# Kernel optimization log

Measured on AMD Instinct MI355X. Metric: run time of the kernel, lower is better.

Reference implementation:

```python
import jax, jax.numpy as jnp
import numpy as np

N_DRUG, N_CELL, N_EDGES = 10000, 20000, 1280000
D_DRUG, D_CELL, BATCH = 384, 3504, 4096


def setup_inputs() -> dict:
    key = jax.random.key(0)
    ks = jax.random.split(key, 24)
    f32 = jnp.float32

    def lin(kw, kb, fan_in, fan_out, bias=True):
        s = 1.0 / np.sqrt(fan_in)
        W = jax.random.uniform(kw, (fan_in, fan_out), f32, -s, s)
        b = jax.random.uniform(kb, (fan_out,), f32, -s, s) if bias else None
        return W, b

    inp = {}
    inp['drug'] = jax.random.randint(ks[0], (BATCH,), 0, N_DRUG)
    inp['cell'] = jax.random.randint(ks[1], (BATCH,), 0, N_CELL)
    # stored node features / edges (constants in the torch module)
    inp['drug_x'] = jax.random.normal(ks[2], (N_DRUG, D_DRUG), f32)
    inp['cell_x'] = jax.random.normal(ks[3], (N_CELL, D_CELL), f32)
    inp['cell_edges'] = jax.random.randint(ks[4], (2, N_EDGES), 0, N_CELL)
    # drug_emb: Linear(384,128)
    inp['demb_W'], inp['demb_b'] = lin(ks[5], ks[6], D_DRUG, 128)
    # SAGEConv(3504,1024): lin_l (with bias) on aggregated, lin_r (no bias) on root
    inp['c1_lW'], inp['c1_lb'] = lin(ks[7], ks[8], D_CELL, 1024)
    inp['c1_rW'], _ = lin(ks[9], ks[9], D_CELL, 1024, bias=False)
    # SAGEConv(1024,256)
    inp['c2_lW'], inp['c2_lb'] = lin(ks[10], ks[11], 1024, 256)
    inp['c2_rW'], _ = lin(ks[12], ks[12], 1024, 256, bias=False)
    inp['reg_W1'], inp['reg_b1'] = lin(ks[13], ks[14], 384, 384)
    inp['reg_W2'], inp['reg_b2'] = lin(ks[15], ks[16], 384, 384)
    inp['reg_W3'], inp['reg_b3'] = lin(ks[17], ks[18], 384, 1)
    return inp


def _sage(x, src, dst, n, lW, lb, rW):
    # PyG SAGEConv, mean aggregation: lin_l(mean_{j in N(i)} x_j) + lin_r(x_i)
    deg = jax.ops.segment_sum(jnp.ones(src.shape[0], x.dtype), dst, num_segments=n)
    agg = jax.ops.segment_sum(x[src], dst, num_segments=n)  # [n, d_in]
    agg = agg / jnp.maximum(deg, 1.0)[:, None]
    return agg @ lW + lb + x @ rW


def reference(drug, cell, drug_x, cell_x, cell_edges,
              demb_W, demb_b, c1_lW, c1_lb, c1_rW, c2_lW, c2_lb, c2_rW,
              reg_W1, reg_b1, reg_W2, reg_b2, reg_W3, reg_b3):
    src, dst = cell_edges[0], cell_edges[1]
    n = cell_x.shape[0]
    # drug branch: Linear + ReLU (dropout = identity at inference)
    d = jax.nn.relu(drug_x @ demb_W + demb_b)                  # [N_drug, 128]
    # cell branch: two SAGEConv + ReLU
    c = jax.nn.relu(_sage(cell_x, src, dst, n, c1_lW, c1_lb, c1_rW))  # [N_cell, 1024]
    c = jax.nn.relu(_sage(c, src, dst, n, c2_lW, c2_lb, c2_rW))       # [N_cell, 256]
    # gather batch rows and concatenate -> [B, 384]
    x = jnp.concatenate([d[drug], c[cell]], axis=-1)
    x = jax.nn.elu(x @ reg_W1 + reg_b1)
    x = jax.nn.elu(x @ reg_W2 + reg_b2)
    return x @ reg_W3 + reg_b3                                 # [B, 1]
```

## Files before the change

### kernel.cpp

```cpp
#include <hip/hip_runtime.h>
#include <hip/hip_bf16.h>

typedef __bf16 bf16x8 __attribute__((ext_vector_type(8)));
typedef float f32x4 __attribute__((ext_vector_type(4)));
typedef float f32x2 __attribute__((ext_vector_type(2)));
typedef unsigned short u16x8 __attribute__((ext_vector_type(8)));

#define N_DRUG   10000
#define N_CELL   20000
#define NEDGE    1280000
#define D_DRUG   384
#define D_CELL   3504
#define D_CELL_P 3520
#define BATCH    4096

typedef unsigned int u32_g __attribute__((address_space(1)));
typedef unsigned int u32_l __attribute__((address_space(3)));

__device__ __forceinline__ void gld_lds16(const void* g, void* l) {
  __builtin_amdgcn_global_load_lds((const u32_g*)g, (u32_l*)l, 16, 0, 0);
}

__device__ __forceinline__ ushort f2bf(float f) {
  union { float f; unsigned u; } v; v.f = f;
  unsigned r = v.u + 0x7fffu + ((v.u >> 16) & 1u);
  return (ushort)(r >> 16);
}
__device__ __forceinline__ float bf2f(ushort h) {
  union { unsigned u; float f; } v; v.u = ((unsigned)h) << 16;
  return v.f;
}

#define S_BARRIER() asm volatile("s_barrier" ::: "memory")
#define VMCNT6()    asm volatile("s_waitcnt vmcnt(6)" ::: "memory")
#define VMCNT0()    asm volatile("s_waitcnt vmcnt(0)" ::: "memory")


__global__ __launch_bounds__(256) void conv_xd(const float* __restrict__ x,
                                               const float* __restrict__ dx,
                                               const int* __restrict__ drug,
                                               ushort* __restrict__ xb,
                                               ushort* __restrict__ adb) {
  const int CXB = (N_CELL * (D_CELL_P / 8)) / 256;
  if (blockIdx.x < CXB) {
    int idx = blockIdx.x * 256 + threadIdx.x;
    const int CH = D_CELL_P / 8;
    int r = idx / CH, c8 = (idx % CH) * 8;
    if (r >= N_CELL) return;
    ushort4 a, b;
    if (c8 < D_CELL) {
      const float* p = x + (size_t)r * D_CELL + c8;
      float4 v0 = *(const float4*)p;
      float4 v1 = *(const float4*)(p + 4);
      a = make_ushort4(f2bf(v0.x), f2bf(v0.y), f2bf(v0.z), f2bf(v0.w));
      b = make_ushort4(f2bf(v1.x), f2bf(v1.y), f2bf(v1.z), f2bf(v1.w));
    } else {
      a = make_ushort4(0,0,0,0); b = make_ushort4(0,0,0,0);
    }
    ushort* q = xb + (size_t)r * D_CELL_P + c8;
    *(ushort4*)q = a; *(ushort4*)(q + 4) = b;
  } else {
    int idx = (blockIdx.x - CXB) * 256 + threadIdx.x;
    int r = idx / 48, c8 = (idx % 48) * 8;
    int g = drug[r];
    const float* p = dx + (size_t)g * D_DRUG + c8;
    float4 v0 = *(const float4*)p, v1 = *(const float4*)(p + 4);
    ushort4 a = make_ushort4(f2bf(v0.x), f2bf(v0.y), f2bf(v0.z), f2bf(v0.w));
    ushort4 b = make_ushort4(f2bf(v1.x), f2bf(v1.y), f2bf(v1.z), f2bf(v1.w));
    ushort* q = adb + (size_t)r * D_DRUG + c8;
    *(ushort4*)q = a; *(ushort4*)(q + 4) = b;
  }
}

__global__ __launch_bounds__(256) void conv_wt_all(
    const float* __restrict__ c1_lW, const float* __restrict__ c1_rW,
    const float* __restrict__ c2_lW, const float* __restrict__ c2_rW,
    const float* __restrict__ demb_W, const float* __restrict__ reg_W1,
    const float* __restrict__ reg_W2,
    ushort* __restrict__ W1t, ushort* __restrict__ W2t, ushort* __restrict__ Wdt,
    ushort* __restrict__ W1rt, ushort* __restrict__ W2rt) {
  int id = blockIdx.x;
  const float *L, *R; int nL, N, Kin, Kp, nkx; ushort* out; int base;
  if (id < 7040)      { base = 0;    L = c1_lW;  R = c1_rW;  nL = 1024; N = 2048; Kin = 3504; Kp = 3520; out = W1t;  nkx = 110; }
  else if (id < 7552) { base = 7040; L = c2_lW;  R = c2_rW;  nL = 256;  N = 512;  Kin = 1024; Kp = 1024; out = W2t;  nkx = 32; }
  else if (id < 7600) { base = 7552; L = demb_W; R = demb_W; nL = 128;  N = 128;  Kin = 384;  Kp = 384;  out = Wdt;  nkx = 12; }
  else if (id < 7744) { base = 7600; L = reg_W1; R = reg_W1; nL = 384;  N = 384;  Kin = 384;  Kp = 384;  out = W1rt; nkx = 12; }
  else                { base = 7744; L = reg_W2; R = reg_W2; nL = 384;  N = 384;  Kin = 384;  Kp = 384;  out = W2rt; nkx = 12; }
  int lid = id - base;
  int k0 = (lid % nkx) * 32, n0 = (lid / nkx) * 32;

  __shared__ float tile[32][33];
  int t = threadIdx.x;
  int tn = t & 31, tk = t >> 5;
  #pragma unroll
  for (int p = 0; p < 4; ++p) {
    int k = k0 + tk + p * 8, n = n0 + tn;
    float v = 0.f;
    if (k < Kin) v = (n < nL) ? L[(size_t)k * nL + n] : R[(size_t)k * (N - nL) + (n - nL)];
    tile[tk + p * 8][tn] = v;
  }
  __syncthreads();
  int wk = t & 31, wn = t >> 5;
  #pragma unroll
  for (int p = 0; p < 4; ++p) {
    int n = n0 + wn + p * 8, k = k0 + wk;
    out[(size_t)n * Kp + k] = f2bf(tile[wk][wn + p * 8]);
  }
}


__global__ void deg_mark(const int* __restrict__ dst, int* __restrict__ deg,
                         const int* __restrict__ cell, int* __restrict__ mark) {
  if (blockIdx.x < 2048) {
    for (int e = blockIdx.x * 256 + threadIdx.x; e < NEDGE; e += 2048 * 256)
      atomicAdd(&deg[dst[e]], 1);
  } else {
    int b = (blockIdx.x - 2048) * 256 + threadIdx.x;
    if (b < BATCH) mark[cell[b]] = 1;
  }
}

__global__ __launch_bounds__(1024) void scan_kernel(const int* __restrict__ deg,
                                                    int* __restrict__ rowptr,
                                                    int* __restrict__ cursor, int n) {
  __shared__ int wsum[16];
  __shared__ int carry_s;
  int t = threadIdx.x, wave = t >> 6, lane = t & 63;
  if (t == 0) carry_s = 0;
  __syncthreads();
  for (int base = 0; base < n; base += 1024) {
    int x = (base + t < n) ? deg[base + t] : 0;
    int v = x;
    #pragma unroll
    for (int off = 1; off < 64; off <<= 1) {
      int u = __shfl_up(v, off, 64);
      if (lane >= off) v += u;
    }
    if (lane == 63) wsum[wave] = v;
    __syncthreads();
    if (wave == 0 && lane < 16) {
      int w = wsum[lane];
      #pragma unroll
      for (int off = 1; off < 16; off <<= 1) {
        int u = __shfl_up(w, off, 64);
        if (lane >= off) w += u;
      }
      wsum[lane] = w;
    }
    __syncthreads();
    int wpre = (wave == 0) ? 0 : wsum[wave - 1];
    int incl = v + wpre;
    int carry = carry_s;
    if (base + t < n) { int ex = carry + incl - x; rowptr[base + t] = ex; cursor[base + t] = ex; }
    __syncthreads();
    if (t == 1023) carry_s = carry + incl;
    __syncthreads();
  }
  if (t == 0) rowptr[n] = carry_s;
}

__global__ void bucket_kernel(const int* __restrict__ src, const int* __restrict__ dst,
                              int* __restrict__ cursor, int* __restrict__ srcs, int n) {
  for (int e = blockIdx.x * blockDim.x + threadIdx.x; e < n; e += gridDim.x * blockDim.x) {
    int p = atomicAdd(&cursor[dst[e]], 1);
    srcs[p] = src[e];
  }
}

template <int EPI, int K>
__global__ __launch_bounds__(512, 2) void gemm8p(const ushort* __restrict__ A,
                                                 const ushort* __restrict__ Bt,
                                                 float* __restrict__ outF,
                                                 ushort* __restrict__ outB,
                                                 int M) {
  constexpr int NK = K / 64;
  __shared__ ushort lds[2][2][32][512];

  const int t = threadIdx.x;
  const int wid = t >> 6, lane = t & 63;
  const int wr = wid >> 2, wc = wid & 3;
  const int brow = blockIdx.y * 256, bcol = blockIdx.x * 256;
  const int fr = lane & 15, kgi = lane >> 4;
  const int slot8 = (fr * 4 + (kgi ^ ((fr >> 1) & 3))) * 8;
  const int srow = lane >> 2;
  const int gsw = ((lane & 3) ^ ((lane >> 3) & 3)) * 8;

  f32x4 acc[8][4];
  #pragma unroll
  for (int m = 0; m < 8; ++m)
    #pragma unroll
    for (int n = 0; n < 4; ++n) acc[m][n] = f32x4{0.f, 0.f, 0.f, 0.f};

  bf16x8 af[4][2], bfg[4][2];

  auto stage = [&](int b, int h, int kt) {
    const ushort* base = (h < 2) ? A : Bt;
    const int rb = (h < 2) ? brow : bcol;
    const int half = h & 1, ab = h >> 1;
    const int k0 = kt * 64;
    #pragma unroll
    for (int j = 0; j < 2; ++j) {
      int c = j * 8 + wid;
      int r16 = half * 8 + (c >> 1), kc = c & 1;
      int row = rb + r16 * 16 + srow;
      if (h < 2) row = row < M ? row : M - 1;
      gld_lds16(base + (size_t)row * K + k0 + kc * 32 + gsw,
                &lds[b][ab][half * 16 + c][0]);
    }
  };

  stage(0, 0, 0); stage(0, 2, 0); stage(0, 3, 0); stage(0, 1, 0);
  stage(1, 0, 1); stage(1, 2, 1); stage(1, 3, 1);
  VMCNT6();
  S_BARRIER();

  for (int kt = 0; kt < NK; ++kt) {
    const int b = kt & 1, nb = b ^ 1;
    const bool dr = (kt >= NK - 2);

    #pragma unroll
    for (int m = 0; m < 4; ++m) {
      af[m][0] = *(const bf16x8*)&lds[b][0][(2 * m + wr) * 2 + 0][slot8];
      af[m][1] = *(const bf16x8*)&lds[b][0][(2 * m + wr) * 2 + 1][slot8];
    }
    #pragma unroll
    for (int n = 0; n < 2; ++n) {
      bfg[n][0] = *(const bf16x8*)&lds[b][1][(4 * n + wc) * 2 + 0][slot8];
      bfg[n][1] = *(const bf16x8*)&lds[b][1][(4 * n + wc) * 2 + 1][slot8];
    }
    if (kt + 1 < NK) stage(nb, 1, kt + 1);
    S_BARRIER();
    __builtin_amdgcn_s_setprio(1);
    #pragma unroll
    for (int m = 0; m < 4; ++m)
      #pragma unroll
      for (int n = 0; n < 2; ++n) {
        acc[m][n] = __builtin_amdgcn_mfma_f32_16x16x32_bf16(af[m][0], bfg[n][0], acc[m][n], 0, 0, 0);
        acc[m][n] = __builtin_amdgcn_mfma_f32_16x16x32_bf16(af[m][1], bfg[n][1], acc[m][n], 0, 0, 0);
      }
    __builtin_amdgcn_s_setprio(0);
    S_BARRIER();

    #pragma unroll
    for (int n = 2; n < 4; ++n) {
      bfg[n][0] = *(const bf16x8*)&lds[b][1][(4 * n + wc) * 2 + 0][slot8];
      bfg[n][1] = *(const bf16x8*)&lds[b][1][(4 * n + wc) * 2 + 1][slot8];
    }
    if (kt + 2 < NK) stage(b, 0, kt + 2);
    S_BARRIER();
    __builtin_amdgcn_s_setprio(1);
    #pragma unroll
    for (int m = 0; m < 4; ++m)
      #pragma unroll
      for (int n = 2; n < 4; ++n) {
        acc[m][n] = __builtin_amdgcn_mfma_f32_16x16x32_bf16(af[m][0], bfg[n][0], acc[m][n], 0, 0, 0);
        acc[m][n] = __builtin_amdgcn_mfma_f32_16x16x32_bf16(af[m][1], bfg[n][1], acc[m][n], 0, 0, 0);
      }
    __builtin_amdgcn_s_setprio(0);
    S_BARRIER();

    #pragma unroll
    for (int m = 0; m < 4; ++m) {
      af[m][0] = *(const bf16x8*)&lds[b][0][(2 * (m + 4) + wr) * 2 + 0][slot8];
      af[m][1] = *(const bf16x8*)&lds[b][0][(2 * (m + 4) + wr) * 2 + 1][slot8];
    }
    if (kt + 2 < NK) stage(b, 2, kt + 2);
    S_BARRIER();
    __builtin_amdgcn_s_setprio(1);
    #pragma unroll
    for (int m = 0; m < 4; ++m)
      #pragma unroll
      for (int n = 0; n < 2; ++n) {
        acc[m + 4][n] = __builtin_amdgcn_mfma_f32_16x16x32_bf16(af[m][0], bfg[n][0], acc[m + 4][n], 0, 0, 0);
        acc[m + 4][n] = __builtin_amdgcn_mfma_f32_16x16x32_bf16(af[m][1], bfg[n][1], acc[m + 4][n], 0, 0, 0);
      }
    __builtin_amdgcn_s_setprio(0);
    S_BARRIER();

    if (kt + 2 < NK) stage(b, 3, kt + 2);
    S_BARRIER();
    __builtin_amdgcn_s_setprio(1);
    #pragma unroll
    for (int m = 0; m < 4; ++m)
      #pragma unroll
      for (int n = 2; n < 4; ++n) {
        acc[m + 4][n] = __builtin_amdgcn_mfma_f32_16x16x32_bf16(af[m][0], bfg[n][0], acc[m + 4][n], 0, 0, 0);
        acc[m + 4][n] = __builtin_amdgcn_mfma_f32_16x16x32_bf16(af[m][1], bfg[n][1], acc[m + 4][n], 0, 0, 0);
      }
    __builtin_amdgcn_s_setprio(0);
    if (dr) { VMCNT0(); } else { VMCNT6(); }
    S_BARRIER();
  }

  unsigned char* o8 = (unsigned char*)outF;
  #pragma unroll
  for (int m = 0; m < 8; ++m)
    #pragma unroll
    for (int n = 0; n < 4; ++n)
      #pragma unroll
      for (int j = 0; j < 4; ++j) {
        int row = brow + (2 * m + wr) * 16 + kgi * 4 + j;
        int col = bcol + (4 * n + wc) * 16 + fr;
        if (row < M) {
          float v = acc[m][n][j];
          if constexpr (EPI == 0) {
            if (col < 1024) {
              int p = __builtin_amdgcn_cvt_pk_fp8_f32(v, v, 0, false);
              o8[(size_t)row * 1024 + col] = (unsigned char)(p & 0xff);
            } else {
              outB[(size_t)row * 1024 + (col - 1024)] = f2bf(v);
            }
          } else {
            outB[(size_t)row * 512 + col] = f2bf(v);
          }
        }
      }
}

template <int EPI>
__global__ __launch_bounds__(256) void gemm_bt(const ushort* __restrict__ A,
                                               const ushort* __restrict__ Bt,
                                               float* __restrict__ outF,
                                               ushort* __restrict__ outB,
                                               const float* __restrict__ bias,
                                               int M, int N, int K, int ldc) {
  __shared__ ushort ldsA[128 * 32];
  __shared__ ushort ldsB[128 * 32];
  const int t = threadIdx.x;
  const int wave = t >> 6, lane = t & 63;
  const int brow = blockIdx.y * 128;
  const int bcol = blockIdx.x * 128;
  const int wr = wave >> 1, wc = wave & 1;

  f32x4 acc[4][4];
  #pragma unroll
  for (int m = 0; m < 4; ++m)
    #pragma unroll
    for (int n = 0; n < 4; ++n) acc[m][n] = f32x4{0.f, 0.f, 0.f, 0.f};

  const int srow = lane >> 2;
  const int gsw  = ((lane & 3) ^ ((lane >> 3) & 3)) * 8;
  const int nk = K >> 5;

  const int fr = lane & 15;
  const int kgi = lane >> 4;
  const int slot = (fr * 4 + (kgi ^ ((fr >> 1) & 3))) * 8;

  for (int kt = 0; kt < nk; ++kt) {
    const int k0 = kt * 32;
    #pragma unroll
    for (int i = 0; i < 2; ++i) {
      int c = i * 4 + wave;
      int arow = brow + c * 16 + srow;
      arow = arow < M ? arow : M - 1;
      gld_lds16(A + (size_t)arow * K + k0 + gsw, ldsA + c * 512);
      int brB = bcol + c * 16 + srow;
      gld_lds16(Bt + (size_t)brB * K + k0 + gsw, ldsB + c * 512);
    }
    __syncthreads();
    bf16x8 af[4], bf[4];
    #pragma unroll
    for (int m = 0; m < 4; ++m) af[m] = *(const bf16x8*)(ldsA + (wr * 4 + m) * 512 + slot);
    #pragma unroll
    for (int n = 0; n < 4; ++n) bf[n] = *(const bf16x8*)(ldsB + (wc * 4 + n) * 512 + slot);
    #pragma unroll
    for (int m = 0; m < 4; ++m)
      #pragma unroll
      for (int n = 0; n < 4; ++n)
        acc[m][n] = __builtin_amdgcn_mfma_f32_16x16x32_bf16(af[m], bf[n], acc[m][n], 0, 0, 0);
    __syncthreads();
  }

  const int fq = lane >> 4;
  #pragma unroll
  for (int m = 0; m < 4; ++m) {
    #pragma unroll
    for (int n = 0; n < 4; ++n) {
      #pragma unroll
      for (int j = 0; j < 4; ++j) {
        int row = brow + wr * 64 + m * 16 + fq * 4 + j;
        int col = bcol + wc * 64 + n * 16 + fr;
        if (row < M) {
          float v = acc[m][n][j];
          if constexpr (EPI == 0) {
            outF[(size_t)row * ldc + col] = v;
          } else if constexpr (EPI == 2) {
            v += bias[col];
            v = fmaxf(v, 0.f);
            outB[(size_t)row * ldc + col] = f2bf(v);
          } else {
            v += bias[col];
            v = v > 0.f ? v : expm1f(v);
            outB[(size_t)row * ldc + col] = f2bf(v);
          }
        }
      }
    }
  }
}


__global__ __launch_bounds__(256) void agg1_c1(const unsigned char* __restrict__ Yl8,
                                               const ushort* __restrict__ Yrb,
                                               const float* __restrict__ lb,
                                               const int* __restrict__ rowptr,
                                               const int* __restrict__ srcs,
                                               ushort* __restrict__ c1b) {
  const int b = blockIdx.x, t = threadIdx.x;
  const int s = b & 7;
  const int i = (b >> 3) * 4 + (t >> 6);
  const int lane = t & 63;
  const int eg = lane >> 3, c8 = lane & 7;
  const int s0 = rowptr[i], s1 = rowptr[i + 1];
  const unsigned char* base = Yl8 + s * 128 + c8 * 16;

  float a[16];
  #pragma unroll
  for (int k = 0; k < 16; ++k) a[k] = 0.f;

  auto accum = [&](uint4 v) {
    const unsigned* w = (const unsigned*)&v;
    #pragma unroll
    for (int q = 0; q < 4; ++q) {
      f32x2 lo = __builtin_amdgcn_cvt_pk_f32_fp8(w[q], false);
      f32x2 hi = __builtin_amdgcn_cvt_pk_f32_fp8(w[q], true);
      a[q * 4 + 0] += lo.x; a[q * 4 + 1] += lo.y;
      a[q * 4 + 2] += hi.x; a[q * 4 + 3] += hi.y;
    }
  };

  int e = s0 + eg;
  for (; e + 8 < s1; e += 16) {
    uint4 vA = *(const uint4*)(base + (size_t)srcs[e] * 1024);
    uint4 vB = *(const uint4*)(base + (size_t)srcs[e + 8] * 1024);
    accum(vA); accum(vB);
  }
  for (; e < s1; e += 8) {
    uint4 v = *(const uint4*)(base + (size_t)srcs[e] * 1024);
    accum(v);
  }
  #pragma unroll
  for (int k = 0; k < 16; ++k) {
    a[k] += __shfl_xor(a[k], 8, 64);
    a[k] += __shfl_xor(a[k], 16, 64);
    a[k] += __shfl_xor(a[k], 32, 64);
  }
  if (eg == 0) {
    float inv = 1.0f / fmaxf((float)(s1 - s0), 1.0f);
    size_t off = (size_t)i * 1024 + s * 128 + c8 * 16;
    u16x8 r0 = *(const u16x8*)(Yrb + off);
    u16x8 r1 = *(const u16x8*)(Yrb + off + 8);
    u16x8 o0, o1;
    #pragma unroll
    for (int k = 0; k < 8; ++k) {
      float v0 = a[k] * inv + lb[s * 128 + c8 * 16 + k] + bf2f(r0[k]);
      float v1 = a[k + 8] * inv + lb[s * 128 + c8 * 16 + 8 + k] + bf2f(r1[k]);
      o0[k] = f2bf(fmaxf(v0, 0.f));
      o1[k] = f2bf(fmaxf(v1, 0.f));
    }
    *(u16x8*)(c1b + off) = o0;
    *(u16x8*)(c1b + off + 8) = o1;
  }
}

__global__ __launch_bounds__(256) void agg2_c2(const ushort* __restrict__ Zb,
                                               const float* __restrict__ lb,
                                               const int* __restrict__ rowptr,
                                               const int* __restrict__ srcs,
                                               const int* __restrict__ mark,
                                               ushort* __restrict__ c2v) {
  int i = blockIdx.x;
  if (!mark[i]) return;
  __shared__ float red[4][32][8];
  int t = threadIdx.x;
  int sub = t >> 5, c = t & 31;
  int wave = t >> 6, lane = t & 63;
  int s0 = rowptr[i], s1 = rowptr[i + 1];
  float a[8] = {0.f, 0.f, 0.f, 0.f, 0.f, 0.f, 0.f, 0.f};
  int e = s0 + sub;
  for (; e + 8 < s1; e += 16) {
    int sA = srcs[e], sB = srcs[e + 8];
    u16x8 vA = *(const u16x8*)(Zb + (size_t)sA * 512 + c * 8);
    u16x8 vB = *(const u16x8*)(Zb + (size_t)sB * 512 + c * 8);
    #pragma unroll
    for (int k = 0; k < 8; ++k) a[k] += bf2f(vA[k]) + bf2f(vB[k]);
  }
  for (; e < s1; e += 8) {
    int src = srcs[e];
    u16x8 v = *(const u16x8*)(Zb + (size_t)src * 512 + c * 8);
    #pragma unroll
    for (int k = 0; k < 8; ++k) a[k] += bf2f(v[k]);
  }
  #pragma unroll
  for (int k = 0; k < 8; ++k) a[k] += __shfl_xor(a[k], 32, 64);
  if (lane < 32) {
    #pragma unroll
    for (int k = 0; k < 8; ++k) red[wave][lane][k] = a[k];
  }
  __syncthreads();
  if (t < 32) {
    float inv = 1.0f / fmaxf((float)(s1 - s0), 1.0f);
    u16x8 r = *(const u16x8*)(Zb + (size_t)i * 512 + 256 + t * 8);
    u16x8 o;
    #pragma unroll
    for (int k = 0; k < 8; ++k) {
      float sum = red[0][t][k] + red[1][t][k] + red[2][t][k] + red[3][t][k];
      float v = sum * inv + lb[t * 8 + k] + bf2f(r[k]);
      o[k] = f2bf(fmaxf(v, 0.f));
    }
    *(u16x8*)(c2v + (size_t)i * 256 + t * 8) = o;
  }
}

__global__ __launch_bounds__(256) void xcat2(const ushort* __restrict__ c2v,
                                             const int* __restrict__ cell,
                                             ushort* __restrict__ xcat) {
  int idx = blockIdx.x * 256 + threadIdx.x;
  int b = idx >> 6, q = idx & 63;
  ushort4 v = *(const ushort4*)(c2v + (size_t)cell[b] * 256 + q * 4);
  *(ushort4*)(xcat + (size_t)b * 384 + 128 + q * 4) = v;
}

__global__ __launch_bounds__(256) void final_k(const ushort* __restrict__ h2,
                                               const float* __restrict__ W3,
                                               const float* __restrict__ b3,
                                               float* __restrict__ out) {
  int row = blockIdx.x * 4 + (threadIdx.x >> 6);
  int lane = threadIdx.x & 63;
  const ushort* p = h2 + (size_t)row * 384;
  float s = 0.f;
  #pragma unroll
  for (int k = lane; k < 384; k += 64) s += bf2f(p[k]) * W3[k];
  #pragma unroll
  for (int off = 32; off; off >>= 1) s += __shfl_xor(s, off, 64);
  if (lane == 0) out[row] = s + b3[0];
}


extern "C" void kernel_launch(void* const* d_in, const int* in_sizes, int n_in,
                              void* d_out, int out_size, void* d_ws, size_t ws_size,
                              hipStream_t stream) {
  (void)in_sizes; (void)n_in; (void)out_size; (void)ws_size;
  const int*   drug   = (const int*)  d_in[0];
  const int*   cell   = (const int*)  d_in[1];
  const float* drug_x = (const float*)d_in[2];
  const float* cell_x = (const float*)d_in[3];
  const int*   edges  = (const int*)  d_in[4];
  const float* demb_W = (const float*)d_in[5];
  const float* demb_b = (const float*)d_in[6];
  const float* c1_lW  = (const float*)d_in[7];
  const float* c1_lb  = (const float*)d_in[8];
  const float* c1_rW  = (const float*)d_in[9];
  const float* c2_lW  = (const float*)d_in[10];
  const float* c2_lb  = (const float*)d_in[11];
  const float* c2_rW  = (const float*)d_in[12];
  const float* reg_W1 = (const float*)d_in[13];
  const float* reg_b1 = (const float*)d_in[14];
  const float* reg_W2 = (const float*)d_in[15];
  const float* reg_b2 = (const float*)d_in[16];
  const float* reg_W3 = (const float*)d_in[17];
  const float* reg_b3 = (const float*)d_in[18];
  float* out = (float*)d_out;

  char* ws = (char*)d_ws;
  size_t off = 0;
  auto alloc = [&](size_t b) { size_t o = off; off += (b + 255) & ~(size_t)255; return o; };
  size_t oXB  = alloc((size_t)N_CELL * D_CELL_P * 2);
  size_t oW1T = alloc((size_t)2048 * D_CELL_P * 2);
  size_t oYL8 = alloc((size_t)N_CELL * 1024);
  size_t oYRB = alloc((size_t)N_CELL * 1024 * 2);
  size_t oW2T = alloc((size_t)512 * 1024 * 2);
  size_t oSRC = alloc((size_t)NEDGE * 4);
  size_t oDEG = alloc((size_t)N_CELL * 4);
  size_t oRPT = alloc((size_t)(N_CELL + 1) * 4);
  size_t oCUR = alloc((size_t)N_CELL * 4);
  size_t oMRK = alloc((size_t)N_CELL * 4);
  size_t oADB = alloc((size_t)BATCH * D_DRUG * 2);
  size_t oWDT = alloc((size_t)128 * 384 * 2);
  size_t oXC  = alloc((size_t)BATCH * 384 * 2);
  size_t oW1R = alloc((size_t)384 * 384 * 2);
  size_t oW2R = alloc((size_t)384 * 384 * 2);
  size_t oH1  = alloc((size_t)BATCH * 384 * 2);
  size_t oH2  = alloc((size_t)BATCH * 384 * 2);

  ushort* Xb   = (ushort*)(ws + oXB);
  ushort* c1b  = (ushort*)(ws + oXB);
  ushort* Zb   = (ushort*)(ws + oXB + 40960000);
  ushort* c2v  = (ushort*)(ws + oXB + 81920000);
  ushort* W1t  = (ushort*)(ws + oW1T);
  unsigned char* Yl8 = (unsigned char*)(ws + oYL8);
  ushort* Yrb  = (ushort*)(ws + oYRB);
  ushort* W2t  = (ushort*)(ws + oW2T);
  int*    srcs = (int*)   (ws + oSRC);
  int*    deg  = (int*)   (ws + oDEG);
  int*    rpt  = (int*)   (ws + oRPT);
  int*    cur  = (int*)   (ws + oCUR);
  int*    mrk  = (int*)   (ws + oMRK);
  ushort* Adb  = (ushort*)(ws + oADB);
  ushort* Wdt  = (ushort*)(ws + oWDT);
  ushort* xcat = (ushort*)(ws + oXC);
  ushort* W1rt = (ushort*)(ws + oW1R);
  ushort* W2rt = (ushort*)(ws + oW2R);
  ushort* h1   = (ushort*)(ws + oH1);
  ushort* h2   = (ushort*)(ws + oH2);

  const int* esrc = edges;
  const int* edst = edges + NEDGE;

  hipMemsetAsync(deg, 0, (size_t)N_CELL * 4, stream);
  hipMemsetAsync(mrk, 0, (size_t)N_CELL * 4, stream);

  deg_mark<<<2064, 256, 0, stream>>>(edst, deg, cell, mrk);
  scan_kernel<<<1, 1024, 0, stream>>>(deg, rpt, cur, N_CELL);
  bucket_kernel<<<2048, 256, 0, stream>>>(esrc, edst, cur, srcs, NEDGE);

  conv_xd<<<(N_CELL * (D_CELL_P / 8)) / 256 + (BATCH * (D_DRUG / 8)) / 256, 256, 0, stream>>>(
      cell_x, drug_x, drug, Xb, Adb);
  conv_wt_all<<<7888, 256, 0, stream>>>(c1_lW, c1_rW, c2_lW, c2_rW, demb_W, reg_W1, reg_W2,
                                        W1t, W2t, Wdt, W1rt, W2rt);

  gemm8p<0, D_CELL_P><<<dim3(2048 / 256, (N_CELL + 255) / 256), 512, 0, stream>>>(
      Xb, W1t, (float*)Yl8, Yrb, N_CELL);
  agg1_c1<<<(N_CELL / 4) * 8, 256, 0, stream>>>(Yl8, Yrb, c1_lb, rpt, srcs, c1b);

  gemm8p<1, 1024><<<dim3(512 / 256, (N_CELL + 255) / 256), 512, 0, stream>>>(
      c1b, W2t, nullptr, Zb, N_CELL);
  agg2_c2<<<N_CELL, 256, 0, stream>>>(Zb, c2_lb, rpt, srcs, mrk, c2v);

  gemm_bt<2><<<dim3(1, BATCH / 128), 256, 0, stream>>>(
      Adb, Wdt, nullptr, xcat, demb_b, BATCH, 128, 384, 384);
  xcat2<<<(BATCH * 64) / 256, 256, 0, stream>>>(c2v, cell, xcat);

  gemm_bt<3><<<dim3(384 / 128, BATCH / 128), 256, 0, stream>>>(
      xcat, W1rt, nullptr, h1, reg_b1, BATCH, 384, 384, 384);
  gemm_bt<3><<<dim3(384 / 128, BATCH / 128), 256, 0, stream>>>(
      h1, W2rt, nullptr, h2, reg_b2, BATCH, 384, 384, 384);
  final_k<<<BATCH / 4, 256, 0, stream>>>(h2, reg_W3, reg_b3, out);
}
```

Measured before the change: 801.0 us.

## Replace 256x256 eight-phase GEMM with 256x128 two-phase pipelined GEMM

Rewrites the main bf16 MFMA GEMM to use 256x128 output tiles per block instead of 256x256. The k-loop now has two MFMA phases with fewer barriers, and each wave computes a 64x64 sub-tile. The aim is to cut barrier and scheduling overhead, lower register pressure and double the grid size for better occupancy. The cost is lower arithmetic intensity, since A tiles are reloaded twice as often. The two memsets are also merged into one by placing the mark array right after the degree array.

```diff
diff --git a/kernel.cpp b/kernel.cpp
--- a/kernel.cpp
+++ b/kernel.cpp
@@ -32,6 +32,7 @@
 }
 
 #define S_BARRIER() asm volatile("s_barrier" ::: "memory")
+#define LGKMCNT0()  asm volatile("s_waitcnt lgkmcnt(0)" ::: "memory")
 #define VMCNT6()    asm volatile("s_waitcnt vmcnt(6)" ::: "memory")
 #define VMCNT0()    asm volatile("s_waitcnt vmcnt(0)" ::: "memory")
 
@@ -168,139 +169,101 @@
 }
 
 template <int EPI, int K>
-__global__ __launch_bounds__(512, 2) void gemm8p(const ushort* __restrict__ A,
+__global__ __launch_bounds__(512, 2) void gemm2p(const ushort* __restrict__ A,
                                                  const ushort* __restrict__ Bt,
                                                  float* __restrict__ outF,
                                                  ushort* __restrict__ outB,
                                                  int M) {
   constexpr int NK = K / 64;
-  __shared__ ushort lds[2][2][32][512];
+  __shared__ ushort lds[2][48][512];
 
   const int t = threadIdx.x;
   const int wid = t >> 6, lane = t & 63;
-  const int wr = wid >> 2, wc = wid & 3;
-  const int brow = blockIdx.y * 256, bcol = blockIdx.x * 256;
+  const int wr = wid >> 1, wc = wid & 1;
+  const int brow = blockIdx.y * 256, bcol = blockIdx.x * 128;
   const int fr = lane & 15, kgi = lane >> 4;
   const int slot8 = (fr * 4 + (kgi ^ ((fr >> 1) & 3))) * 8;
   const int srow = lane >> 2;
   const int gsw = ((lane & 3) ^ ((lane >> 3) & 3)) * 8;
 
-  f32x4 acc[8][4];
-  #pragma unroll
-  for (int m = 0; m < 8; ++m)
+  f32x4 acc[4][4];
+  #pragma unroll
+  for (int m = 0; m < 4; ++m)
     #pragma unroll
     for (int n = 0; n < 4; ++n) acc[m][n] = f32x4{0.f, 0.f, 0.f, 0.f};
 
-  bf16x8 af[4][2], bfg[4][2];
-
   auto stage = [&](int b, int h, int kt) {
-    const ushort* base = (h < 2) ? A : Bt;
-    const int rb = (h < 2) ? brow : bcol;
-    const int half = h & 1, ab = h >> 1;
     const int k0 = kt * 64;
     #pragma unroll
     for (int j = 0; j < 2; ++j) {
       int c = j * 8 + wid;
-      int r16 = half * 8 + (c >> 1), kc = c & 1;
-      int row = rb + r16 * 16 + srow;
-      if (h < 2) row = row < M ? row : M - 1;
-      gld_lds16(base + (size_t)row * K + k0 + kc * 32 + gsw,
-                &lds[b][ab][half * 16 + c][0]);
+      int kc = c & 1;
+      if (h < 2) {
+        int r16 = h * 8 + (c >> 1);
+        int row = brow + r16 * 16 + srow;
+        row = row < M ? row : M - 1;
+        gld_lds16(A + (size_t)row * K + k0 + kc * 32 + gsw, &lds[b][r16 * 2 + kc][0]);
+      } else {
+        int r16b = c >> 1;
+        int row = bcol + r16b * 16 + srow;
+        gld_lds16(Bt + (size_t)row * K + k0 + kc * 32 + gsw, &lds[b][32 + r16b * 2 + kc][0]);
+      }
     }
   };
 
-  stage(0, 0, 0); stage(0, 2, 0); stage(0, 3, 0); stage(0, 1, 0);
-  stage(1, 0, 1); stage(1, 2, 1); stage(1, 3, 1);
+  stage(0, 0, 0); stage(0, 1, 0); stage(0, 2, 0);
+  stage(1, 0, 1); stage(1, 1, 1); stage(1, 2, 1);
   VMCNT6();
   S_BARRIER();
 
   for (int kt = 0; kt < NK; ++kt) {
-    const int b = kt & 1, nb = b ^ 1;
-    const bool dr = (kt >= NK - 2);
+    const int b = kt & 1;
+    const bool dr = (kt + 2 >= NK);
+    bf16x8 af[4][2], bf[4][2];
 
     #pragma unroll
     for (int m = 0; m < 4; ++m) {
-      af[m][0] = *(const bf16x8*)&lds[b][0][(2 * m + wr) * 2 + 0][slot8];
-      af[m][1] = *(const bf16x8*)&lds[b][0][(2 * m + wr) * 2 + 1][slot8];
-    }
-    #pragma unroll
-    for (int n = 0; n < 2; ++n) {
-      bfg[n][0] = *(const bf16x8*)&lds[b][1][(4 * n + wc) * 2 + 0][slot8];
-      bfg[n][1] = *(const bf16x8*)&lds[b][1][(4 * n + wc) * 2 + 1][slot8];
-    }
-    if (kt + 1 < NK) stage(nb, 1, kt + 1);
-    S_BARRIER();
+      af[m][0] = *(const bf16x8*)&lds[b][(wr * 4 + m) * 2 + 0][slot8];
+      af[m][1] = *(const bf16x8*)&lds[b][(wr * 4 + m) * 2 + 1][slot8];
+    }
+    #pragma unroll
+    for (int n = 0; n < 4; ++n)
+      bf[n][0] = *(const bf16x8*)&lds[b][32 + (wc * 4 + n) * 2 + 0][slot8];
     __builtin_amdgcn_s_setprio(1);
     #pragma unroll
     for (int m = 0; m < 4; ++m)
       #pragma unroll
-      for (int n = 0; n < 2; ++n) {
-        acc[m][n] = __builtin_amdgcn_mfma_f32_16x16x32_bf16(af[m][0], bfg[n][0], acc[m][n], 0, 0, 0);
-        acc[m][n] = __builtin_amdgcn_mfma_f32_16x16x32_bf16(af[m][1], bfg[n][1], acc[m][n], 0, 0, 0);
-      }
+      for (int n = 0; n < 4; ++n)
+        acc[m][n] = __builtin_amdgcn_mfma_f32_16x16x32_bf16(af[m][0], bf[n][0], acc[m][n], 0, 0, 0);
     __builtin_amdgcn_s_setprio(0);
+
+    #pragma unroll
+    for (int n = 0; n < 4; ++n)
+      bf[n][1] = *(const bf16x8*)&lds[b][32 + (wc * 4 + n) * 2 + 1][slot8];
+    LGKMCNT0();
     S_BARRIER();
-
-    #pragma unroll
-    for (int n = 2; n < 4; ++n) {
-      bfg[n][0] = *(const bf16x8*)&lds[b][1][(4 * n + wc) * 2 + 0][slot8];
-      bfg[n][1] = *(const bf16x8*)&lds[b][1][(4 * n + wc) * 2 + 1][slot8];
-    }
-    if (kt + 2 < NK) stage(b, 0, kt + 2);
-    S_BARRIER();
+    if (!dr) { stage(b, 0, kt + 2); stage(b, 1, kt + 2); stage(b, 2, kt + 2); }
     __builtin_amdgcn_s_setprio(1);
     #pragma unroll
     for (int m = 0; m < 4; ++m)
       #pragma unroll
-      for (int n = 2; n < 4; ++n) {
-        acc[m][n] = __builtin_amdgcn_mfma_f32_16x16x32_bf16(af[m][0], bfg[n][0], acc[m][n], 0, 0, 0);
-        acc[m][n] = __builtin_amdgcn_mfma_f32_16x16x32_bf16(af[m][1], bfg[n][1], acc[m][n], 0, 0, 0);
-      }
-    __builtin_amdgcn_s_setprio(0);
-    S_BARRIER();
-
-    #pragma unroll
-    for (int m = 0; m < 4; ++m) {
-      af[m][0] = *(const bf16x8*)&lds[b][0][(2 * (m + 4) + wr) * 2 + 0][slot8];
-      af[m][1] = *(const bf16x8*)&lds[b][0][(2 * (m + 4) + wr) * 2 + 1][slot8];
-    }
-    if (kt + 2 < NK) stage(b, 2, kt + 2);
-    S_BARRIER();
-    __builtin_amdgcn_s_setprio(1);
-    #pragma unroll
-    for (int m = 0; m < 4; ++m)
-      #pragma unroll
-      for (int n = 0; n < 2; ++n) {
-        acc[m + 4][n] = __builtin_amdgcn_mfma_f32_16x16x32_bf16(af[m][0], bfg[n][0], acc[m + 4][n], 0, 0, 0);
-        acc[m + 4][n] = __builtin_amdgcn_mfma_f32_16x16x32_bf16(af[m][1], bfg[n][1], acc[m + 4][n], 0, 0, 0);
-      }
-    __builtin_amdgcn_s_setprio(0);
-    S_BARRIER();
-
-    if (kt + 2 < NK) stage(b, 3, kt + 2);
-    S_BARRIER();
-    __builtin_amdgcn_s_setprio(1);
-    #pragma unroll
-    for (int m = 0; m < 4; ++m)
-      #pragma unroll
-      for (int n = 2; n < 4; ++n) {
-        acc[m + 4][n] = __builtin_amdgcn_mfma_f32_16x16x32_bf16(af[m][0], bfg[n][0], acc[m + 4][n], 0, 0, 0);
-        acc[m + 4][n] = __builtin_amdgcn_mfma_f32_16x16x32_bf16(af[m][1], bfg[n][1], acc[m + 4][n], 0, 0, 0);
-      }
+      for (int n = 0; n < 4; ++n)
+        acc[m][n] = __builtin_amdgcn_mfma_f32_16x16x32_bf16(af[m][1], bf[n][1], acc[m][n], 0, 0, 0);
     __builtin_amdgcn_s_setprio(0);
     if (dr) { VMCNT0(); } else { VMCNT6(); }
     S_BARRIER();
   }
 
   unsigned char* o8 = (unsigned char*)outF;
-  #pragma unroll
-  for (int m = 0; m < 8; ++m)
+  const int fq = lane >> 4;
+  #pragma unroll
+  for (int m = 0; m < 4; ++m)
     #pragma unroll
     for (int n = 0; n < 4; ++n)
       #pragma unroll
       for (int j = 0; j < 4; ++j) {
-        int row = brow + (2 * m + wr) * 16 + kgi * 4 + j;
-        int col = bcol + (4 * n + wc) * 16 + fr;
+        int row = brow + wr * 64 + m * 16 + fq * 4 + j;
+        int col = bcol + wc * 64 + n * 16 + fr;
         if (row < M) {
           float v = acc[m][n][j];
           if constexpr (EPI == 0) {
@@ -572,9 +535,9 @@
   size_t oW2T = alloc((size_t)512 * 1024 * 2);
   size_t oSRC = alloc((size_t)NEDGE * 4);
   size_t oDEG = alloc((size_t)N_CELL * 4);
+  size_t oMRK = alloc((size_t)N_CELL * 4);
   size_t oRPT = alloc((size_t)(N_CELL + 1) * 4);
   size_t oCUR = alloc((size_t)N_CELL * 4);
-  size_t oMRK = alloc((size_t)N_CELL * 4);
   size_t oADB = alloc((size_t)BATCH * D_DRUG * 2);
   size_t oWDT = alloc((size_t)128 * 384 * 2);
   size_t oXC  = alloc((size_t)BATCH * 384 * 2);
@@ -593,9 +556,9 @@
   ushort* W2t  = (ushort*)(ws + oW2T);
   int*    srcs = (int*)   (ws + oSRC);
   int*    deg  = (int*)   (ws + oDEG);
+  int*    mrk  = (int*)   (ws + oMRK);
   int*    rpt  = (int*)   (ws + oRPT);
   int*    cur  = (int*)   (ws + oCUR);
-  int*    mrk  = (int*)   (ws + oMRK);
   ushort* Adb  = (ushort*)(ws + oADB);
   ushort* Wdt  = (ushort*)(ws + oWDT);
   ushort* xcat = (ushort*)(ws + oXC);
@@ -607,8 +570,7 @@
   const int* esrc = edges;
   const int* edst = edges + NEDGE;
 
-  hipMemsetAsync(deg, 0, (size_t)N_CELL * 4, stream);
-  hipMemsetAsync(mrk, 0, (size_t)N_CELL * 4, stream);
+  hipMemsetAsync(deg, 0, (oMRK - oDEG) + (size_t)N_CELL * 4, stream);
 
   deg_mark<<<2064, 256, 0, stream>>>(edst, deg, cell, mrk);
   scan_kernel<<<1, 1024, 0, stream>>>(deg, rpt, cur, N_CELL);
@@ -619,11 +581,11 @@
   conv_wt_all<<<7888, 256, 0, stream>>>(c1_lW, c1_rW, c2_lW, c2_rW, demb_W, reg_W1, reg_W2,
                                         W1t, W2t, Wdt, W1rt, W2rt);
 
-  gemm8p<0, D_CELL_P><<<dim3(2048 / 256, (N_CELL + 255) / 256), 512, 0, stream>>>(
+  gemm2p<0, D_CELL_P><<<dim3(2048 / 128, (N_CELL + 255) / 256), 512, 0, stream>>>(
       Xb, W1t, (float*)Yl8, Yrb, N_CELL);
   agg1_c1<<<(N_CELL / 4) * 8, 256, 0, stream>>>(Yl8, Yrb, c1_lb, rpt, srcs, c1b);
 
-  gemm8p<1, 1024><<<dim3(512 / 256, (N_CELL + 255) / 256), 512, 0, stream>>>(
+  gemm2p<1, 1024><<<dim3(512 / 128, (N_CELL + 255) / 256), 512, 0, stream>>>(
       c1b, W2t, nullptr, Zb, N_CELL);
   agg2_c2<<<N_CELL, 256, 0, stream>>>(Zb, c2_lb, rpt, srcs, mrk, c2v);
 
```

Result: slower. 848.4 us (+5.9%).
